# Performance work log

Hardware: AMD Instinct MI355X
Metric: run time of the kernel (lower is better)

## Reference

```python
import jax, jax.numpy as jnp
import numpy as np


def setup_inputs() -> dict:
    key = jax.random.key(0)
    k1, k2, k3, k4, k5 = jax.random.split(key, 5)
    n_mol, n_atm, d_feat, n_props = 128, 64, 384, 64
    n_ref = n_mol * n_atm  # 8192 reference atoms (flattened)
    # element labels in {1,2,3,4} (e.g. H,C,N,O); all atoms nondummy (Z>0)
    Z_ref = jax.random.randint(k1, (n_mol, n_atm), 1, 5)
    Z = jax.random.randint(k2, (n_mol, n_atm), 1, 5)
    # descriptors, scaled so the poly kernel K^expK stays O(1)
    scale = 1.0 / np.sqrt(d_feat).astype(np.float32)
    X_ref = jax.random.normal(k3, (n_ref, d_feat), jnp.float32) * scale
    desc = jax.random.normal(k4, (n_mol, n_atm, d_feat), jnp.float32) * scale
    Alpha = jax.random.normal(k5, (n_props, n_ref), jnp.float32)
    return {"Alpha": Alpha, "X_ref": X_ref, "desc": desc,
            "Z_ref": Z_ref, "Z": Z, "expK": 2}


def reference(Alpha, X_ref, desc, Z_ref, Z, expK):
    # Faithful dense formulation of the per-element gather/matmul/scatter:
    # y[p, j] = sum_i Alpha[p, i] * (X_ref[i] . X_in[j])^expK * [Z_ref[i] == Z[j]]
    # Each query atom j belongs to exactly one element, so the masked dense
    # kernel reproduces the grouped computation exactly (same flat ordering
    # as torch's molecule-major concatenation).
    d_feat = X_ref.shape[-1]
    X_in = desc.reshape(-1, d_feat)                      # [N_in, d]
    K = jnp.power(X_ref @ X_in.T, expK)                  # [N_ref, N_in]
    mask = Z_ref.reshape(-1)[:, None] == Z.reshape(-1)[None, :]
    y = Alpha @ jnp.where(mask, K, jnp.float32(0.0))     # [n_props, N_in]
    return y
```

## Files before the change

kernel.cpp:

```cpp
#include <hip/hip_runtime.h>
#include <hip/hip_bf16.h>
#include <stdint.h>


typedef __attribute__((ext_vector_type(8))) short bf16x8;
typedef __attribute__((ext_vector_type(4))) float f32x4;
typedef __attribute__((ext_vector_type(4))) unsigned int u32x4;

#define DFEAT  384
#define NREF   8192
#define NIN    8192
#define NPROPS 64
#define BJ 128
#define BI 128
#define BK 64
#define KSTEPS (DFEAT / BK)
#define CAP    8704
#define NSTRIP (CAP / BJ)

__device__ __forceinline__ void gload_lds16(const void* g, void* l) {
  __builtin_amdgcn_global_load_lds(
      (const __attribute__((address_space(1))) void*)g,
      (__attribute__((address_space(3))) void*)l,
      16, 0, 0);
}

__device__ __forceinline__ unsigned short bfbits(float f) {
  __hip_bfloat16 h = __float2bfloat16(f);
  return __builtin_bit_cast(unsigned short, h);
}

__device__ __forceinline__ float pwr(float s, int expK) {
  if (expK == 2) return s * s;
  float r = 1.0f;
  for (int e = 0; e < expK; ++e) r *= s;
  return r;
}

__global__ __launch_bounds__(256) void partition_kernel(
    const int* __restrict__ Zin, int* __restrict__ perm, int* __restrict__ goff) {
  __shared__ int cnt[256][4];
  __shared__ int gstart[4];
  __shared__ int gtot[4];
  const int t = threadIdx.x;
  const int base = t * 32;

  int c[4] = {0, 0, 0, 0};
  int zloc[32];
  #pragma unroll
  for (int e = 0; e < 32; ++e) {
    zloc[e] = (Zin[base + e] - 1) & 3;
    ++c[zloc[e]];
  }
  #pragma unroll
  for (int b = 0; b < 4; ++b) cnt[t][b] = c[b];
  __syncthreads();

  const int w = t >> 6, l = t & 63;
  {
    int v0 = cnt[4 * l + 0][w], v1 = cnt[4 * l + 1][w];
    int v2 = cnt[4 * l + 2][w], v3 = cnt[4 * l + 3][w];
    int s = v0 + v1 + v2 + v3;
    int inc = s;
    #pragma unroll
    for (int d = 1; d < 64; d <<= 1) {
      int o = __shfl_up(inc, d, 64);
      if (l >= d) inc += o;
    }
    const int excl = inc - s;
    cnt[4 * l + 0][w] = excl;
    cnt[4 * l + 1][w] = excl + v0;
    cnt[4 * l + 2][w] = excl + v0 + v1;
    cnt[4 * l + 3][w] = excl + v0 + v1 + v2;
    if (l == 63) gtot[w] = inc;
  }
  __syncthreads();

  if (t == 0) {
    int off = 0;
    #pragma unroll
    for (int b = 0; b < 4; ++b) {
      gstart[b] = off; goff[b] = off;
      off += ((gtot[b] + 127) >> 7) << 7;
    }
    goff[4] = off;
  }
  __syncthreads();

  for (int s = t; s < CAP; s += 256) perm[s] = -1;
  __syncthreads();

  int pos[4];
  #pragma unroll
  for (int b = 0; b < 4; ++b) pos[b] = gstart[b] + cnt[t][b];
  #pragma unroll
  for (int e = 0; e < 32; ++e) {
    const int z = zloc[e];
    perm[pos[z]++] = base + e;
  }
}

__global__ void gather_x_bf16(const float* __restrict__ in,
                              const int* __restrict__ perm,
                              __hip_bfloat16* __restrict__ out) {
  const int idx = blockIdx.x * blockDim.x + threadIdx.x;
  const int per_row = DFEAT / 4;
  const int slot = idx / per_row;
  const int c4 = (idx % per_row) * 4;
  const int src = perm[slot];
  ushort4 o = make_ushort4(0, 0, 0, 0);
  if (src >= 0) {
    float4 v = *reinterpret_cast<const float4*>(in + (size_t)src * DFEAT + c4);
    o.x = bfbits(v.x); o.y = bfbits(v.y); o.z = bfbits(v.z); o.w = bfbits(v.w);
  }
  *reinterpret_cast<ushort4*>(out + (size_t)slot * DFEAT + c4) = o;
}

__global__ void gather_alpha_perm(const float* __restrict__ in,
                                  const int* __restrict__ perm,
                                  __hip_bfloat16* __restrict__ out) {
  const int t = blockIdx.x * blockDim.x + threadIdx.x;
  const int per_row = CAP / 4;
  const int p  = t / per_row;
  const int c4 = t % per_row;
  const int b   = c4 >> 3;
  const int g   = c4 & 7;
  const int l4g = g >> 1;
  const int eh  = g & 1;
  ushort4 o;
  unsigned short* op = &o.x;
  #pragma unroll
  for (int r = 0; r < 4; ++r) {
    const int slot = b * 32 + eh * 16 + l4g * 4 + r;
    const int src = perm[slot];
    op[r] = (src >= 0) ? bfbits(in[(size_t)p * NREF + src]) : (unsigned short)0;
  }
  *reinterpret_cast<ushort4*>(out + (size_t)p * CAP + b * 32 + l4g * 8 + eh * 4) = o;
}

__global__ void reduce_scatter(const float* __restrict__ partial,
                               const int* __restrict__ permj,
                               float* __restrict__ out, int nsplit) {
  const int idx = blockIdx.x * blockDim.x + threadIdx.x;
  const int p = idx / CAP;
  const int slot = idx % CAP;
  const int dst = permj[slot];
  if (dst < 0) return;
  float s = 0.f;
  for (int sp = 0; sp < nsplit; ++sp)
    s += partial[(size_t)sp * NPROPS * CAP + (size_t)p * CAP + slot];
  out[(size_t)p * NIN + dst] = s;
}

__global__ __launch_bounds__(256, 2) void fused_poly_kernel(
    const __hip_bfloat16* __restrict__ Xr,
    const __hip_bfloat16* __restrict__ Xi,
    const __hip_bfloat16* __restrict__ Abp,
    const int* __restrict__ ioff,
    const int* __restrict__ joff,
    const int* __restrict__ expKp,
    float* __restrict__ partial,
    int nsplit)
{
  const int j0 = blockIdx.x * BJ;
  const int split = blockIdx.y;

  int grp = 0;
  grp += (j0 >= joff[1]);
  grp += (j0 >= joff[2]);
  grp += (j0 >= joff[3]);
  const int ibase = ioff[grp];
  const int ntiles_g = (ioff[grp + 1] - ibase) / BI;

  const int tb = ntiles_g / nsplit;
  const int rem = ntiles_g % nsplit;
  const int ntiles = tb + (split < rem ? 1 : 0);
  const int tile_begin = split * tb + (split < rem ? split : rem);

  const int tid  = threadIdx.x;
  const int wid  = tid >> 6;
  const int lane = tid & 63;
  const int l15  = lane & 15;
  const int l4   = lane >> 4;
  const int s7   = l15 & 7;
  const int wi   = wid >> 1;
  const int wj   = wid & 1;

  __shared__ alignas(16) __hip_bfloat16 lA[2][BI * BK];
  __shared__ alignas(16) __hip_bfloat16 lB[2][BJ * BK];

  const int expK = *expKp;

  const int srow = lane >> 3;
  const int scol = ((lane & 7) ^ srow) * 8;

  auto stage = [&](int buf, int i0s, int kks) {
    #pragma unroll
    for (int q = 0; q < 4; ++q) {
      const int c = wid * 4 + q;
      const int grow = c * 8 + srow;
      const size_t gc = (size_t)kks * BK + scol;
      gload_lds16(Xr + (size_t)(i0s + grow) * DFEAT + gc, &lA[buf][c * 512]);
      gload_lds16(Xi + (size_t)(j0  + grow) * DFEAT + gc, &lB[buf][c * 512]);
    }
  };

  f32x4 accO[4][4];
  #pragma unroll
  for (int a = 0; a < 4; ++a)
    #pragma unroll
    for (int n = 0; n < 4; ++n)
      accO[a][n] = (f32x4){0.f, 0.f, 0.f, 0.f};

  if (ntiles > 0) {
    int cur = 0;
    stage(0, ibase + tile_begin * BI, 0);
    asm volatile("s_waitcnt vmcnt(0)" ::: "memory");
    __builtin_amdgcn_s_barrier();

    for (int t = 0; t < ntiles; ++t) {
      const int i0 = ibase + (tile_begin + t) * BI;

      f32x4 acc[4][4];
      #pragma unroll
      for (int m = 0; m < 4; ++m)
        #pragma unroll
        for (int n = 0; n < 4; ++n)
          acc[m][n] = (f32x4){0.f, 0.f, 0.f, 0.f};

      for (int kk = 0; kk < KSTEPS; ++kk) {
        if (kk < KSTEPS - 1) {
          stage(cur ^ 1, i0, kk + 1);
        } else if (t < ntiles - 1) {
          stage(cur ^ 1, i0 + BI, 0);
        }

        __builtin_amdgcn_s_setprio(1);
        #pragma unroll
        for (int kap = 0; kap < 2; ++kap) {
          bf16x8 aF[4], bF[4];
          #pragma unroll
          for (int m = 0; m < 4; ++m) {
            const int rA = wi * 64 + m * 16 + l15;
            aF[m] = *reinterpret_cast<const bf16x8*>(
                (char*)(&lA[cur][0]) + rA * 128 + (((kap * 4 + l4) ^ s7) << 4));
          }
          #pragma unroll
          for (int n = 0; n < 4; ++n) {
            const int rB = wj * 64 + n * 16 + l15;
            bF[n] = *reinterpret_cast<const bf16x8*>(
                (char*)(&lB[cur][0]) + rB * 128 + (((kap * 4 + l4) ^ s7) << 4));
          }
          #pragma unroll
          for (int m = 0; m < 4; ++m)
            #pragma unroll
            for (int n = 0; n < 4; ++n)
              acc[m][n] = __builtin_amdgcn_mfma_f32_16x16x32_bf16(
                  aF[m], bF[n], acc[m][n], 0, 0, 0);
        }
        __builtin_amdgcn_s_setprio(0);
        asm volatile("s_waitcnt vmcnt(0) lgkmcnt(0)" ::: "memory");
        __builtin_amdgcn_s_barrier();
        cur ^= 1;
      }

      bf16x8 aP[2][4];
      #pragma unroll
      for (int ks = 0; ks < 2; ++ks)
        #pragma unroll
        for (int a = 0; a < 4; ++a)
          aP[ks][a] = *reinterpret_cast<const bf16x8*>(
              Abp + (size_t)(a * 16 + l15) * CAP + i0 + wi * 64 + ks * 32 + l4 * 8);

      uint32_t lov[4][4], hiv[4][4];
      #pragma unroll
      for (int m = 0; m < 4; ++m) {
        #pragma unroll
        for (int n = 0; n < 4; ++n) {
          const float p0 = pwr(acc[m][n][0], expK);
          const float p1 = pwr(acc[m][n][1], expK);
          const float p2 = pwr(acc[m][n][2], expK);
          const float p3 = pwr(acc[m][n][3], expK);
          lov[m][n] = (uint32_t)bfbits(p0) | ((uint32_t)bfbits(p1) << 16);
          hiv[m][n] = (uint32_t)bfbits(p2) | ((uint32_t)bfbits(p3) << 16);
        }
      }

      __builtin_amdgcn_s_setprio(1);
      #pragma unroll
      for (int ks = 0; ks < 2; ++ks) {
        #pragma unroll
        for (int n = 0; n < 4; ++n) {
          u32x4 tw;
          tw[0] = lov[2 * ks][n];
          tw[1] = hiv[2 * ks][n];
          tw[2] = lov[2 * ks + 1][n];
          tw[3] = hiv[2 * ks + 1][n];
          const bf16x8 bP = __builtin_bit_cast(bf16x8, tw);
          #pragma unroll
          for (int a = 0; a < 4; ++a)
            accO[a][n] = __builtin_amdgcn_mfma_f32_16x16x32_bf16(
                aP[ks][a], bP, accO[a][n], 0, 0, 0);
        }
      }
      __builtin_amdgcn_s_setprio(0);
    }
  }

  float* rb = (float*)lA;
  if (wi == 1) {
    #pragma unroll
    for (int a = 0; a < 4; ++a)
      #pragma unroll
      for (int n = 0; n < 4; ++n)
        #pragma unroll
        for (int r = 0; r < 4; ++r)
          rb[wj * 4096 + (a * 16 + l4 * 4 + r) * 64 + n * 16 + l15] =
              accO[a][n][r];
  }
  __syncthreads();
  if (wi == 0) {
    float* po = partial + (size_t)split * NPROPS * CAP;
    #pragma unroll
    for (int a = 0; a < 4; ++a)
      #pragma unroll
      for (int n = 0; n < 4; ++n)
        #pragma unroll
        for (int r = 0; r < 4; ++r) {
          const int p = a * 16 + l4 * 4 + r;
          const int jl = wj * 64 + n * 16 + l15;
          po[(size_t)p * CAP + j0 + jl] =
              accO[a][n][r] + rb[wj * 4096 + p * 64 + n * 16 + l15];
        }
  }
}

extern "C" void kernel_launch(void* const* d_in, const int* in_sizes, int n_in,
                              void* d_out, int out_size, void* d_ws, size_t ws_size,
                              hipStream_t stream) {
  (void)in_sizes; (void)n_in; (void)out_size;
  const float* Alpha = (const float*)d_in[0];
  const float* X_ref = (const float*)d_in[1];
  const float* desc  = (const float*)d_in[2];
  const int*   Z_ref = (const int*)d_in[3];
  const int*   Z     = (const int*)d_in[4];
  const int*   expK  = (const int*)d_in[5];
  float* out = (float*)d_out;

  char* ws = (char*)d_ws;
  size_t off = 0;
  auto alloc = [&](size_t b) { void* p = ws + off; off = (off + b + 255) & ~255ULL; return p; };

  int* perm_i = (int*)alloc(CAP * 4);
  int* perm_j = (int*)alloc(CAP * 4);
  int* ioff   = (int*)alloc(8 * 4);
  int* joff   = (int*)alloc(8 * 4);
  __hip_bfloat16* Xr_g = (__hip_bfloat16*)alloc((size_t)CAP * DFEAT * 2);
  __hip_bfloat16* Xi_g = (__hip_bfloat16*)alloc((size_t)CAP * DFEAT * 2);
  __hip_bfloat16* Ab_g = (__hip_bfloat16*)alloc((size_t)NPROPS * CAP * 2);

  int nsplit = 8;
  while (nsplit > 1 && off + (size_t)nsplit * NPROPS * CAP * 4 > ws_size) nsplit >>= 1;
  float* partial = (float*)alloc((size_t)nsplit * NPROPS * CAP * 4);

  partition_kernel<<<1, 256, 0, stream>>>(Z_ref, perm_i, ioff);
  partition_kernel<<<1, 256, 0, stream>>>(Z,     perm_j, joff);

  { int nt = CAP * (DFEAT / 4);
    gather_x_bf16<<<dim3(nt / 256), 256, 0, stream>>>(X_ref, perm_i, Xr_g); }
  { int nt = CAP * (DFEAT / 4);
    gather_x_bf16<<<dim3(nt / 256), 256, 0, stream>>>(desc, perm_j, Xi_g); }
  { int nt = NPROPS * (CAP / 4);
    gather_alpha_perm<<<dim3(nt / 256), 256, 0, stream>>>(Alpha, perm_i, Ab_g); }

  fused_poly_kernel<<<dim3(NSTRIP, nsplit), 256, 0, stream>>>(
      Xr_g, Xi_g, Ab_g, ioff, joff, expK, partial, nsplit);

  reduce_scatter<<<dim3(NPROPS * CAP / 256), 256, 0, stream>>>(
      partial, perm_j, out, nsplit);
}
```

Before: 83.02 us.

## Merge launches, remap blocks across XCDs, early-exit empty strips, relax waits

Folds the two partition launches into one two-block kernel and the three gather launches into a single gather_all kernel, cutting launch count and the gaps between small kernels. The fused GEMM now uses a flat grid with an XCD-aware block remap and returns early for strips beyond the padded query count. The vmcnt wait is moved to just before compute and loosened to vmcnt(8), so the next stage's loads stay in flight. The vmcnt(8) count must match the number of loads each stage issues, or the pipeline could read stale LDS.

```diff
diff --git a/kernel.cpp b/kernel.cpp
--- a/kernel.cpp
+++ b/kernel.cpp
@@ -37,8 +37,14 @@
   return r;
 }
 
-__global__ __launch_bounds__(256) void partition_kernel(
-    const int* __restrict__ Zin, int* __restrict__ perm, int* __restrict__ goff) {
+__global__ __launch_bounds__(256) void partition2_kernel(
+    const int* __restrict__ Za, const int* __restrict__ Zb,
+    int* __restrict__ perma, int* __restrict__ permb,
+    int* __restrict__ goffa, int* __restrict__ goffb) {
+  const int* Zin = blockIdx.x ? Zb : Za;
+  int* perm = blockIdx.x ? permb : perma;
+  int* goff = blockIdx.x ? goffb : goffa;
+
   __shared__ int cnt[256][4];
   __shared__ int gstart[4];
   __shared__ int gtot[4];
@@ -100,42 +106,51 @@
   }
 }
 
-__global__ void gather_x_bf16(const float* __restrict__ in,
-                              const int* __restrict__ perm,
-                              __hip_bfloat16* __restrict__ out) {
-  const int idx = blockIdx.x * blockDim.x + threadIdx.x;
-  const int per_row = DFEAT / 4;
-  const int slot = idx / per_row;
-  const int c4 = (idx % per_row) * 4;
-  const int src = perm[slot];
-  ushort4 o = make_ushort4(0, 0, 0, 0);
-  if (src >= 0) {
-    float4 v = *reinterpret_cast<const float4*>(in + (size_t)src * DFEAT + c4);
-    o.x = bfbits(v.x); o.y = bfbits(v.y); o.z = bfbits(v.z); o.w = bfbits(v.w);
-  }
-  *reinterpret_cast<ushort4*>(out + (size_t)slot * DFEAT + c4) = o;
-}
-
-__global__ void gather_alpha_perm(const float* __restrict__ in,
-                                  const int* __restrict__ perm,
-                                  __hip_bfloat16* __restrict__ out) {
-  const int t = blockIdx.x * blockDim.x + threadIdx.x;
-  const int per_row = CAP / 4;
-  const int p  = t / per_row;
-  const int c4 = t % per_row;
-  const int b   = c4 >> 3;
-  const int g   = c4 & 7;
-  const int l4g = g >> 1;
-  const int eh  = g & 1;
-  ushort4 o;
-  unsigned short* op = &o.x;
-  #pragma unroll
-  for (int r = 0; r < 4; ++r) {
-    const int slot = b * 32 + eh * 16 + l4g * 4 + r;
+#define XSEC (CAP * (DFEAT / 4) / 256)
+__global__ void gather_all(const float* __restrict__ Xr_in,
+                           const float* __restrict__ Xi_in,
+                           const float* __restrict__ Al_in,
+                           const int* __restrict__ perm_i,
+                           const int* __restrict__ perm_j,
+                           __hip_bfloat16* __restrict__ Xr_g,
+                           __hip_bfloat16* __restrict__ Xi_g,
+                           __hip_bfloat16* __restrict__ Ab_g) {
+  const int b = blockIdx.x;
+  if (b < 2 * XSEC) {
+    const bool isA = (b < XSEC);
+    const float* in = isA ? Xr_in : Xi_in;
+    const int* perm = isA ? perm_i : perm_j;
+    __hip_bfloat16* out = isA ? Xr_g : Xi_g;
+    const int idx = (isA ? b : b - XSEC) * 256 + threadIdx.x;
+    const int per_row = DFEAT / 4;
+    const int slot = idx / per_row;
+    const int c4 = (idx % per_row) * 4;
     const int src = perm[slot];
-    op[r] = (src >= 0) ? bfbits(in[(size_t)p * NREF + src]) : (unsigned short)0;
-  }
-  *reinterpret_cast<ushort4*>(out + (size_t)p * CAP + b * 32 + l4g * 8 + eh * 4) = o;
+    ushort4 o = make_ushort4(0, 0, 0, 0);
+    if (src >= 0) {
+      float4 v = *reinterpret_cast<const float4*>(in + (size_t)src * DFEAT + c4);
+      o.x = bfbits(v.x); o.y = bfbits(v.y); o.z = bfbits(v.z); o.w = bfbits(v.w);
+    }
+    *reinterpret_cast<ushort4*>(out + (size_t)slot * DFEAT + c4) = o;
+  } else {
+    const int t = (b - 2 * XSEC) * 256 + threadIdx.x;
+    const int per_row = CAP / 4;
+    const int p  = t / per_row;
+    const int c4 = t % per_row;
+    const int blk = c4 >> 3;
+    const int g   = c4 & 7;
+    const int l4g = g >> 1;
+    const int eh  = g & 1;
+    ushort4 o;
+    unsigned short* op = &o.x;
+    #pragma unroll
+    for (int r = 0; r < 4; ++r) {
+      const int slot = blk * 32 + eh * 16 + l4g * 4 + r;
+      const int src = perm_i[slot];
+      op[r] = (src >= 0) ? bfbits(Al_in[(size_t)p * NREF + src]) : (unsigned short)0;
+    }
+    *reinterpret_cast<ushort4*>(Ab_g + (size_t)p * CAP + blk * 32 + l4g * 8 + eh * 4) = o;
+  }
 }
 
 __global__ void reduce_scatter(const float* __restrict__ partial,
@@ -160,10 +175,15 @@
     const int* __restrict__ joff,
     const int* __restrict__ expKp,
     float* __restrict__ partial,
-    int nsplit)
+    int nsplit, int chunk)
 {
-  const int j0 = blockIdx.x * BJ;
-  const int split = blockIdx.y;
+  const int flat = blockIdx.x;
+  const int newflat = (flat & 7) * chunk + (flat >> 3);
+  const int strip = newflat / nsplit;
+  const int split = newflat % nsplit;
+  const int j0 = strip * BJ;
+
+  if (j0 >= joff[4]) return;
 
   int grp = 0;
   grp += (j0 >= joff[1]);
@@ -215,8 +235,6 @@
   if (ntiles > 0) {
     int cur = 0;
     stage(0, ibase + tile_begin * BI, 0);
-    asm volatile("s_waitcnt vmcnt(0)" ::: "memory");
-    __builtin_amdgcn_s_barrier();
 
     for (int t = 0; t < ntiles; ++t) {
       const int i0 = ibase + (tile_begin + t) * BI;
@@ -229,11 +247,17 @@
           acc[m][n] = (f32x4){0.f, 0.f, 0.f, 0.f};
 
       for (int kk = 0; kk < KSTEPS; ++kk) {
+        bool staged = true;
         if (kk < KSTEPS - 1) {
           stage(cur ^ 1, i0, kk + 1);
         } else if (t < ntiles - 1) {
           stage(cur ^ 1, i0 + BI, 0);
+        } else {
+          staged = false;
         }
+        if (staged) asm volatile("s_waitcnt vmcnt(8)" ::: "memory");
+        else        asm volatile("s_waitcnt vmcnt(0)" ::: "memory");
+        __builtin_amdgcn_s_barrier();
 
         __builtin_amdgcn_s_setprio(1);
         #pragma unroll
@@ -259,7 +283,7 @@
                   aF[m], bF[n], acc[m][n], 0, 0, 0);
         }
         __builtin_amdgcn_s_setprio(0);
-        asm volatile("s_waitcnt vmcnt(0) lgkmcnt(0)" ::: "memory");
+        asm volatile("s_waitcnt lgkmcnt(0)" ::: "memory");
         __builtin_amdgcn_s_barrier();
         cur ^= 1;
       }
@@ -363,18 +387,15 @@
   while (nsplit > 1 && off + (size_t)nsplit * NPROPS * CAP * 4 > ws_size) nsplit >>= 1;
   float* partial = (float*)alloc((size_t)nsplit * NPROPS * CAP * 4);
 
-  partition_kernel<<<1, 256, 0, stream>>>(Z_ref, perm_i, ioff);
-  partition_kernel<<<1, 256, 0, stream>>>(Z,     perm_j, joff);
-
-  { int nt = CAP * (DFEAT / 4);
-    gather_x_bf16<<<dim3(nt / 256), 256, 0, stream>>>(X_ref, perm_i, Xr_g); }
-  { int nt = CAP * (DFEAT / 4);
-    gather_x_bf16<<<dim3(nt / 256), 256, 0, stream>>>(desc, perm_j, Xi_g); }
-  { int nt = NPROPS * (CAP / 4);
-    gather_alpha_perm<<<dim3(nt / 256), 256, 0, stream>>>(Alpha, perm_i, Ab_g); }
-
-  fused_poly_kernel<<<dim3(NSTRIP, nsplit), 256, 0, stream>>>(
-      Xr_g, Xi_g, Ab_g, ioff, joff, expK, partial, nsplit);
+  partition2_kernel<<<dim3(2), 256, 0, stream>>>(
+      Z_ref, Z, perm_i, perm_j, ioff, joff);
+
+  gather_all<<<dim3(2 * XSEC + NPROPS * (CAP / 4) / 256), 256, 0, stream>>>(
+      X_ref, desc, Alpha, perm_i, perm_j, Xr_g, Xi_g, Ab_g);
+
+  const int grid = NSTRIP * nsplit;
+  fused_poly_kernel<<<dim3(grid), 256, 0, stream>>>(
+      Xr_g, Xi_g, Ab_g, ioff, joff, expK, partial, nsplit, grid / 8);
 
   reduce_scatter<<<dim3(NPROPS * CAP / 256), 256, 0, stream>>>(
       partial, perm_j, out, nsplit);
```

After: 77.67 us. 6.5% less time.
